# Kernel optimization log

Measured on AMD Instinct MI355X. Metric: run time of the kernel, lower is better.

The kernel has to match this reference:

```python
import jax, jax.numpy as jnp
import numpy as np

DIM = 512
CHUNK = 64
LN_EPS = 1e-5


def setup_inputs() -> dict:
    key = jax.random.key(0)
    ks = jax.random.split(key, 9)
    B, S, D = 4, 4096, DIM
    x = jax.random.normal(ks[0], (B, S, D), dtype=jnp.float32)
    # Linear weights stored as [in, out] (equivalent to torch W.T)
    W_omega = jax.random.normal(ks[1], (D, D), dtype=jnp.float32) / np.sqrt(D)
    b_omega = jnp.zeros((D,), dtype=jnp.float32)
    log_scale = jnp.full((D,), np.log(0.1), dtype=jnp.float32)
    ln_gamma = jnp.ones((4 * D,), dtype=jnp.float32)
    ln_beta = jnp.zeros((4 * D,), dtype=jnp.float32)
    W1 = jax.random.normal(ks[2], (4 * D, 2 * D), dtype=jnp.float32) / np.sqrt(4 * D)
    b1 = jnp.zeros((2 * D,), dtype=jnp.float32)
    W2 = jax.random.normal(ks[3], (2 * D, D), dtype=jnp.float32) / np.sqrt(2 * D)
    b2 = jnp.zeros((D,), dtype=jnp.float32)
    return {"x": x, "W_omega": W_omega, "b_omega": b_omega, "log_scale": log_scale,
            "ln_gamma": ln_gamma, "ln_beta": ln_beta, "W1": W1, "b1": b1, "W2": W2, "b2": b2}


def reference(x, W_omega, b_omega, log_scale, ln_gamma, ln_beta, W1, b1, W2, b2):
    B, S, D = x.shape
    C = CHUNK
    # S chosen as multiple of C, so pad_len == 0 (matches torch no-pad branch)
    N = S // C
    omega = x @ W_omega + b_omega                      # [B,S,D]
    oc = omega.reshape(B, N, C, D)
    xc = x.reshape(B, N, C, D)
    pos = jnp.arange(1, C + 1, dtype=x.dtype)          # [C]
    pos_scale = (1.0 / jnp.sqrt(pos))[None, None, :, None]
    scale = jnp.exp(log_scale)
    phi = jnp.cumsum(oc * scale * pos_scale, axis=2)   # [B,N,C,D]
    cos_phi = jnp.cos(phi)
    sin_phi = jnp.sin(phi)
    cr = xc * cos_phi                                   # content modulated real
    ci = xc * sin_phi                                   # content modulated imag
    pos_norm = pos[None, None, :, None]
    mr = jnp.cumsum(cr, axis=2) / pos_norm              # memory real
    mi = jnp.cumsum(ci, axis=2) / pos_norm              # memory imag
    rr = mr * cos_phi + mi * sin_phi                    # retrieved real
    ri = mi * cos_phi - mr * sin_phi                    # retrieved imag
    ctx = jnp.concatenate([cr.reshape(B, S, D), ci.reshape(B, S, D),
                           rr.reshape(B, S, D), ri.reshape(B, S, D)], axis=-1)  # [B,S,4D]
    mu = jnp.mean(ctx, axis=-1, keepdims=True)
    var = jnp.mean((ctx - mu) ** 2, axis=-1, keepdims=True)
    h = (ctx - mu) / jnp.sqrt(var + LN_EPS) * ln_gamma + ln_beta
    h = h @ W1 + b1
    h = jax.nn.gelu(h, approximate=False)               # torch GELU default = exact erf
    out = h @ W2 + b2                                   # dropout is identity at eval
    return x + out
```

## Files before the change

kernel.cpp:

```cpp
#include <hip/hip_runtime.h>
#include <hip/hip_bf16.h>
#include <math.h>


typedef __bf16 bf16x8 __attribute__((ext_vector_type(8)));
typedef __bf16 bf16x4 __attribute__((ext_vector_type(4)));
typedef __bf16 bf16x2 __attribute__((ext_vector_type(2)));
typedef float  f32x4  __attribute__((ext_vector_type(4)));

typedef __attribute__((address_space(1))) void* gas_ptr;
typedef __attribute__((address_space(3))) void* las_ptr;

__device__ __forceinline__ void load_lds16(const void* g, void* l) {
    __builtin_amdgcn_global_load_lds((gas_ptr)g, (las_ptr)l, 16, 0, 0);
}

__device__ __forceinline__ void transpose_tile(const float* __restrict__ in,
                                               __bf16* __restrict__ out,
                                               int K, int N, int bx, int by,
                                               float (*tile)[33])
{
    const int tid = threadIdx.x;
    const int tx = tid & 31, ty = tid >> 5;
    const int n0 = bx * 32, k0 = by * 32;
    #pragma unroll
    for (int i = 0; i < 32; i += 8)
        tile[ty + i][tx] = in[(size_t)(k0 + ty + i) * N + n0 + tx];
    __syncthreads();
    #pragma unroll
    for (int i = 0; i < 32; i += 8)
        out[(size_t)(n0 + ty + i) * K + k0 + tx] = (__bf16)tile[tx][ty + i];
}

__global__ __launch_bounds__(256)
void prep_kernel(const float* __restrict__ x, __bf16* __restrict__ xb,
                 const float* __restrict__ W_omega, __bf16* __restrict__ womT,
                 const float* __restrict__ W1, __bf16* __restrict__ w1T,
                 const float* __restrict__ W2, __bf16* __restrict__ w2T)
{
    __shared__ float tile[32][33];
    const int bid = blockIdx.x;
    if (bid < 8192) {
        int i = bid * 256 + threadIdx.x;
        float4 v = ((const float4*)x)[i];
        bf16x4 o = { (__bf16)v.x, (__bf16)v.y, (__bf16)v.z, (__bf16)v.w };
        ((bf16x4*)xb)[i] = o;
    } else if (bid < 8448) {
        int t = bid - 8192;
        transpose_tile(W_omega, womT, 512, 512, t & 15, t >> 4, tile);
    } else if (bid < 10496) {
        int t = bid - 8448;
        transpose_tile(W1, w1T, 2048, 1024, t & 31, t >> 5, tile);
    } else {
        int t = bid - 10496;
        transpose_tile(W2, w2T, 1024, 512, t & 15, t >> 4, tile);
    }
}

template<int MODE>
__global__ __launch_bounds__(256)
void gemm_kernel(const __bf16* __restrict__ A, const __bf16* __restrict__ Bt,
                 const float* __restrict__ bias, const __bf16* __restrict__ resid,
                 void* __restrict__ out, int M, int N, int K)
{
    __shared__ __bf16 As[2][128 * 64];
    __shared__ __bf16 Bs[2][128 * 64];

    const int tid     = threadIdx.x;
    const int tiles_n = N >> 7;
    const int ln_tn   = __ffs(tiles_n) - 1;
    const int per_m   = (M >> 7) >> 3;

    const int xcd = blockIdx.x & 7;
    const int j   = blockIdx.x >> 3;
    const int tile_m = (xcd * per_m + (j >> ln_tn)) << 7;
    const int tile_n = (j & (tiles_n - 1)) << 7;

    const int wave = tid >> 6;
    const int lane = tid & 63;

    const int srow = lane >> 3;
    const int scol = ((lane & 7) ^ srow) << 3;

    const __bf16* Ags = A  + (size_t)(tile_m + wave * 32 + srow) * K + scol;
    const __bf16* Bgs = Bt + (size_t)(tile_n + wave * 32 + srow) * K + scol;

    const int m0 = (wave >> 1) << 6;
    const int n0 = (wave & 1) << 6;
    const int lr = lane & 15;
    const int q  = lane >> 4;
    const int l7 = lane & 7;
    const int fc0 = ((0 + q) ^ l7) << 3;
    const int fc1 = ((4 + q) ^ l7) << 3;

    f32x4 acc[4][4];
    #pragma unroll
    for (int i = 0; i < 4; ++i)
        #pragma unroll
        for (int jj = 0; jj < 4; ++jj)
            acc[i][jj] = (f32x4){0.f, 0.f, 0.f, 0.f};

    const int nIter = K >> 6;

    #pragma unroll
    for (int c = 0; c < 4; ++c) {
        load_lds16(Ags + (size_t)(c * 8) * K, &As[0][(wave * 32 + c * 8) * 64]);
        load_lds16(Bgs + (size_t)(c * 8) * K, &Bs[0][(wave * 32 + c * 8) * 64]);
    }

    for (int it = 0; it < nIter; ++it) {
        const int cur = it & 1;
        __syncthreads();
        if (it + 1 < nIter) {
            const int nk = (it + 1) << 6;
            #pragma unroll
            for (int c = 0; c < 4; ++c) {
                load_lds16(Ags + nk + (size_t)(c * 8) * K, &As[cur ^ 1][(wave * 32 + c * 8) * 64]);
                load_lds16(Bgs + nk + (size_t)(c * 8) * K, &Bs[cur ^ 1][(wave * 32 + c * 8) * 64]);
            }
        }

        const __bf16* as = As[cur];
        const __bf16* bs = Bs[cur];
        {
            bf16x8 af[4], bq[4];
            #pragma unroll
            for (int i = 0; i < 4; ++i)
                af[i] = *(const bf16x8*)&as[(m0 + i * 16 + lr) * 64 + fc0];
            #pragma unroll
            for (int jj = 0; jj < 4; ++jj)
                bq[jj] = *(const bf16x8*)&bs[(n0 + jj * 16 + lr) * 64 + fc0];
            #pragma unroll
            for (int i = 0; i < 4; ++i)
                #pragma unroll
                for (int jj = 0; jj < 4; ++jj)
                    acc[i][jj] = __builtin_amdgcn_mfma_f32_16x16x32_bf16(af[i], bq[jj], acc[i][jj], 0, 0, 0);
        }
        {
            bf16x8 af[4], bq[4];
            #pragma unroll
            for (int i = 0; i < 4; ++i)
                af[i] = *(const bf16x8*)&as[(m0 + i * 16 + lr) * 64 + fc1];
            #pragma unroll
            for (int jj = 0; jj < 4; ++jj)
                bq[jj] = *(const bf16x8*)&bs[(n0 + jj * 16 + lr) * 64 + fc1];
            #pragma unroll
            for (int i = 0; i < 4; ++i)
                #pragma unroll
                for (int jj = 0; jj < 4; ++jj)
                    acc[i][jj] = __builtin_amdgcn_mfma_f32_16x16x32_bf16(af[i], bq[jj], acc[i][jj], 0, 0, 0);
        }
    }

    const int orow0 = tile_m + m0 + (q << 2);
    const int ocol0 = tile_n + n0 + lr;
    #pragma unroll
    for (int i = 0; i < 4; ++i) {
        #pragma unroll
        for (int jj = 0; jj < 4; ++jj) {
            const int col = ocol0 + jj * 16;
            const float bv = bias[col];
            #pragma unroll
            for (int r = 0; r < 4; ++r) {
                const int row = orow0 + i * 16 + r;
                float v = acc[i][jj][r] + bv;
                size_t idx = (size_t)row * N + col;
                if (MODE == 0) {
                    ((__bf16*)out)[idx] = (__bf16)v;
                } else if (MODE == 1) {
                    float g = 0.5f * v * (1.0f + erff(v * 0.70710678118654752f));
                    ((__bf16*)out)[idx] = (__bf16)g;
                } else {
                    ((float*)out)[idx] = v + (float)resid[idx];
                }
            }
        }
    }
}

__global__ __launch_bounds__(512)
void scan_ln_kernel(const __bf16* __restrict__ xb, const __bf16* __restrict__ omega,
                    const float* __restrict__ log_scale,
                    const float* __restrict__ gamma, const float* __restrict__ beta,
                    __bf16* __restrict__ ctx)
{
    const int chunk = blockIdx.x;
    const int d     = threadIdx.x;
    const int lane  = d & 63, wv = d >> 6;
    const size_t base = (size_t)chunk * 64 * 512;

    const float scale = expf(log_scale[d]);
    const float g0 = gamma[d], g1 = gamma[512 + d], g2 = gamma[1024 + d], g3 = gamma[1536 + d];
    const float e0 = beta[d],  e1 = beta[512 + d],  e2 = beta[1024 + d],  e3 = beta[1536 + d];

    float phi = 0.f, scr = 0.f, sci = 0.f;
    __shared__ float red[2][16];

    float om_n = (float)omega[base + d];
    float xv_n = (float)xb[base + d];

    for (int c = 0; c < 64; ++c) {
        const float om = om_n;
        const float xv = xv_n;
        if (c < 63) {
            om_n = (float)omega[base + (size_t)(c + 1) * 512 + d];
            xv_n = (float)xb[base + (size_t)(c + 1) * 512 + d];
        }
        phi += om * scale * rsqrtf((float)(c + 1));
        float sp, cp;
        __sincosf(phi, &sp, &cp);
        const float cr = xv * cp, ci = xv * sp;
        scr += cr; sci += ci;
        const float inv = 1.0f / (float)(c + 1);
        const float mr = scr * inv, mi = sci * inv;
        const float rr = mr * cp + mi * sp;
        const float ri = mi * cp - mr * sp;

        float s  = cr + ci + rr + ri;
        float s2 = cr * cr + ci * ci + rr * rr + ri * ri;
        #pragma unroll
        for (int o = 32; o > 0; o >>= 1) {
            s  += __shfl_down(s, o);
            s2 += __shfl_down(s2, o);
        }
        if (lane == 0) { red[c & 1][wv] = s; red[c & 1][8 + wv] = s2; }
        __syncthreads();
        float S = 0.f, S2 = 0.f;
        #pragma unroll
        for (int i = 0; i < 8; ++i) { S += red[c & 1][i]; S2 += red[c & 1][8 + i]; }
        const float mu   = S * (1.0f / 2048.0f);
        const float var  = S2 * (1.0f / 2048.0f) - mu * mu;
        const float rstd = rsqrtf(var + 1e-5f);

        const size_t ob = ((size_t)chunk * 64 + c) * 2048;
        ctx[ob + d]        = (__bf16)(((cr - mu) * rstd) * g0 + e0);
        ctx[ob + 512 + d]  = (__bf16)(((ci - mu) * rstd) * g1 + e1);
        ctx[ob + 1024 + d] = (__bf16)(((rr - mu) * rstd) * g2 + e2);
        ctx[ob + 1536 + d] = (__bf16)(((ri - mu) * rstd) * g3 + e3);
    }
}

extern "C" void kernel_launch(void* const* d_in, const int* in_sizes, int n_in,
                              void* d_out, int out_size, void* d_ws, size_t ws_size,
                              hipStream_t stream)
{
    const float* x         = (const float*)d_in[0];
    const float* W_omega   = (const float*)d_in[1];
    const float* b_omega   = (const float*)d_in[2];
    const float* log_scale = (const float*)d_in[3];
    const float* ln_gamma  = (const float*)d_in[4];
    const float* ln_beta   = (const float*)d_in[5];
    const float* W1        = (const float*)d_in[6];
    const float* b1        = (const float*)d_in[7];
    const float* W2        = (const float*)d_in[8];
    const float* b2        = (const float*)d_in[9];
    float* out = (float*)d_out;

    char* ws = (char*)d_ws;
    __bf16* xb    = (__bf16*)(ws);
    __bf16* womT  = (__bf16*)(ws + 16777216);
    __bf16* w1T   = (__bf16*)(ws + 17301504);
    __bf16* w2T   = (__bf16*)(ws + 21495808);
    __bf16* omega = (__bf16*)(ws + 22544384);
    __bf16* hbuf  = (__bf16*)(ws + 22544384);
    __bf16* ctx   = (__bf16*)(ws + 56098816);

    prep_kernel<<<11008, 256, 0, stream>>>(x, xb, W_omega, womT, W1, w1T, W2, w2T);

    gemm_kernel<0><<<512, 256, 0, stream>>>(xb, womT, b_omega, nullptr, omega, 16384, 512, 512);

    scan_ln_kernel<<<256, 512, 0, stream>>>(xb, omega, log_scale, ln_gamma, ln_beta, ctx);

    gemm_kernel<1><<<1024, 256, 0, stream>>>(ctx, w1T, b1, nullptr, hbuf, 16384, 1024, 2048);

    gemm_kernel<2><<<512, 256, 0, stream>>>(hbuf, w2T, b2, xb, out, 16384, 512, 1024);
}
```

Baseline: 274.4 us.

## Add 256x256-tile multistage bf16 GEMM kernel for the W1 projection

Adds a new GEMM kernel with 256x256 output tiles, 512 threads and a 4-slot LDS ring. It fills the ring with direct global-to-LDS loads, uses XOR-swizzled fragment reads and raises wave priority around the MFMA block. The kernel replaces the generic GEMM for the largest matmul (ctx times W1 with fused GELU) and launches exactly 256 blocks with an XCD-aware tile mapping. The goal is more operand reuse per LDS byte and better overlap of loads with MFMA work. The cost is 128KB of LDS per block, which allows only one block per CU, and much higher register pressure from the 8x4 accumulator tile.

```diff
diff --git a/kernel.cpp b/kernel.cpp
--- a/kernel.cpp
+++ b/kernel.cpp
@@ -178,6 +178,118 @@
     }
 }
 
+template<int MODE>
+__global__ __launch_bounds__(512, 2)
+void gemm256_kernel(const __bf16* __restrict__ A, const __bf16* __restrict__ Bt,
+                    const float* __restrict__ bias, void* __restrict__ out,
+                    int M, int N, int K)
+{
+    __shared__ __bf16 As[4][256 * 32];
+    __shared__ __bf16 Bs[4][256 * 32];
+
+    const int tid  = threadIdx.x;
+    const int wv   = tid >> 6;
+    const int lane = tid & 63;
+    const int wm   = wv >> 2;
+    const int wn   = wv & 3;
+
+    const int tiles_n = N >> 8;
+    const int ln_tn   = __ffs(tiles_n) - 1;
+    const int per_m   = (M >> 8) >> 3;
+
+    const int xcd = blockIdx.x & 7;
+    const int j   = blockIdx.x >> 3;
+    const int tile_m = (xcd * per_m + (j >> ln_tn)) << 8;
+    const int tile_n = (j & (tiles_n - 1)) << 8;
+
+    const int srow = 16 * wv + (lane >> 2);
+    const int sig8 = (((lane & 3) ^ ((lane >> 3) & 3)) << 3);
+
+    const __bf16* Ag = A  + (size_t)(tile_m + srow) * K + sig8;
+    const __bf16* Bg = Bt + (size_t)(tile_n + srow) * K + sig8;
+    const size_t rowK128 = (size_t)128 * K;
+    const int lbase = wv * 512;
+
+    const int lr    = lane & 15;
+    const int q4    = lane >> 4;
+    const int fslot = ((q4 ^ ((lane >> 1) & 3)) << 3);
+    const int arow0 = wm * 128 + lr;
+    const int brow0 = wn * 64 + lr;
+
+    f32x4 acc[8][4];
+    #pragma unroll
+    for (int i = 0; i < 8; ++i)
+        #pragma unroll
+        for (int jj = 0; jj < 4; ++jj)
+            acc[i][jj] = (f32x4){0.f, 0.f, 0.f, 0.f};
+
+    const int NKS = K >> 5;
+
+    auto stage = [&](int ks) {
+        const int slot = ks & 3;
+        const __bf16* ag = Ag + (ks << 5);
+        const __bf16* bg = Bg + (ks << 5);
+        load_lds16(ag,           &As[slot][lbase]);
+        load_lds16(ag + rowK128, &As[slot][4096 + lbase]);
+        load_lds16(bg,           &Bs[slot][lbase]);
+        load_lds16(bg + rowK128, &Bs[slot][4096 + lbase]);
+    };
+
+    if (0 < NKS) stage(0);
+    if (1 < NKS) stage(1);
+    if (2 < NKS) stage(2);
+
+    for (int ks = 0; ks < NKS; ++ks) {
+        if (ks + 2 < NKS)      asm volatile("s_waitcnt vmcnt(8)" ::: "memory");
+        else if (ks + 1 < NKS) asm volatile("s_waitcnt vmcnt(4)" ::: "memory");
+        else                   asm volatile("s_waitcnt vmcnt(0)" ::: "memory");
+        __builtin_amdgcn_s_barrier();
+        asm volatile("" ::: "memory");
+
+        if (ks + 3 < NKS) stage(ks + 3);
+
+        const __bf16* as = As[ks & 3];
+        const __bf16* bs = Bs[ks & 3];
+        bf16x8 af[8], bq[4];
+        #pragma unroll
+        for (int i = 0; i < 8; ++i)
+            af[i] = *(const bf16x8*)&as[(arow0 + i * 16) * 32 + fslot];
+        #pragma unroll
+        for (int jj = 0; jj < 4; ++jj)
+            bq[jj] = *(const bf16x8*)&bs[(brow0 + jj * 16) * 32 + fslot];
+
+        __builtin_amdgcn_s_setprio(1);
+        #pragma unroll
+        for (int i = 0; i < 8; ++i)
+            #pragma unroll
+            for (int jj = 0; jj < 4; ++jj)
+                acc[i][jj] = __builtin_amdgcn_mfma_f32_16x16x32_bf16(af[i], bq[jj], acc[i][jj], 0, 0, 0);
+        __builtin_amdgcn_s_setprio(0);
+    }
+
+    const int orow0 = tile_m + wm * 128 + (q4 << 2);
+    const int ocol0 = tile_n + wn * 64 + lr;
+    #pragma unroll
+    for (int i = 0; i < 8; ++i) {
+        #pragma unroll
+        for (int jj = 0; jj < 4; ++jj) {
+            const int col = ocol0 + jj * 16;
+            const float bv = bias[col];
+            #pragma unroll
+            for (int r = 0; r < 4; ++r) {
+                const int row = orow0 + i * 16 + r;
+                float v = acc[i][jj][r] + bv;
+                if (MODE == 1) {
+                    float g = 0.5f * v * (1.0f + erff(v * 0.70710678118654752f));
+                    ((__bf16*)out)[(size_t)row * N + col] = (__bf16)g;
+                } else {
+                    ((__bf16*)out)[(size_t)row * N + col] = (__bf16)v;
+                }
+            }
+        }
+    }
+}
+
 __global__ __launch_bounds__(512)
 void scan_ln_kernel(const __bf16* __restrict__ xb, const __bf16* __restrict__ omega,
                     const float* __restrict__ log_scale,
@@ -271,7 +383,7 @@
 
     scan_ln_kernel<<<256, 512, 0, stream>>>(xb, omega, log_scale, ln_gamma, ln_beta, ctx);
 
-    gemm_kernel<1><<<1024, 256, 0, stream>>>(ctx, w1T, b1, nullptr, hbuf, 16384, 1024, 2048);
+    gemm256_kernel<1><<<256, 512, 0, stream>>>(ctx, w1T, b1, hbuf, 16384, 1024, 2048);
 
     gemm_kernel<2><<<512, 256, 0, stream>>>(hbuf, w2T, b2, xb, out, 16384, 512, 1024);
 }
```

Result: slower. 285.1 us (+3.9%).

## Use 256x256-tile 512-thread GEMM with LDS double buffering for W1 projection

Applied to the files above, without the earlier changes.

Adds a new GEMM kernel with 256x256 output tiles, 8 waves per block, double-buffered global-to-LDS async loads with XOR swizzle, interleaved staging and MFMA phases, and XCD-aware tile mapping. It replaces the previous 128-tile GEMM for the large LN-to-W1 projection with fused GELU, aiming to raise arithmetic intensity and overlap loads with compute. The larger tile reduces the grid to 256 blocks at one block per CU, so occupancy is low and correctness depends on the hand-written swizzle and sync scheme.

```diff
diff --git a/kernel.cpp b/kernel.cpp
--- a/kernel.cpp
+++ b/kernel.cpp
@@ -178,6 +178,157 @@
     }
 }
 
+template<int MODE>
+__global__ __launch_bounds__(512, 1)
+void gemm256_kernel(const __bf16* __restrict__ A, const __bf16* __restrict__ Bt,
+                    const float* __restrict__ bias, void* __restrict__ out,
+                    int M, int N, int K)
+{
+    __shared__ __bf16 As[2 * 2 * 128 * 64];
+    __shared__ __bf16 Bs[2 * 2 * 128 * 64];
+
+    const int tid  = threadIdx.x;
+    const int wv   = tid >> 6;
+    const int lane = tid & 63;
+    const int wm   = wv >> 2;
+    const int wn   = wv & 3;
+
+    const int tiles_n = N >> 8;
+    const int ln_tn   = __ffs(tiles_n) - 1;
+    const int per_m   = (M >> 8) >> 3;
+
+    const int xcd = blockIdx.x & 7;
+    const int j   = blockIdx.x >> 3;
+    const int tile_m = (xcd * per_m + (j >> ln_tn)) << 8;
+    const int tile_n = (j & (tiles_n - 1)) << 8;
+
+    const int srow8 = lane >> 3;
+    const int sig8  = ((lane & 7) ^ srow8) << 3;
+    const __bf16* AgBase = A  + (size_t)(tile_m + wv * 8 + srow8) * K + sig8;
+    const __bf16* BgBase = Bt + (size_t)(tile_n + wv * 8 + srow8) * K + sig8;
+
+    const int lr = lane & 15;
+    const int q  = lane >> 4;
+    const unsigned ldsA0 = (unsigned)(size_t)(las_ptr)&As[0];
+    const unsigned ldsB0 = (unsigned)(size_t)(las_ptr)&Bs[0];
+    const unsigned chs   = (unsigned)((q ^ (lr & 7)) << 4);
+    const unsigned aA0b0 = ldsA0 + (unsigned)(wm * 16384 + lr * 128) + chs;
+    const unsigned aA1b0 = aA0b0 ^ 64;
+    const unsigned aA0b1 = aA0b0 + 32768;
+    const unsigned aA1b1 = aA1b0 + 32768;
+    const unsigned aB0b0 = ldsB0 + (unsigned)((wn >> 1) * 16384 + ((wn & 1) * 64 + lr) * 128) + chs;
+    const unsigned aB1b0 = aB0b0 ^ 64;
+    const unsigned aB0b1 = aB0b0 + 32768;
+    const unsigned aB1b1 = aB1b0 + 32768;
+
+    f32x4 acc[8][4];
+    #pragma unroll
+    for (int i = 0; i < 8; ++i)
+        #pragma unroll
+        for (int jj = 0; jj < 4; ++jj)
+            acc[i][jj] = (f32x4){0.f, 0.f, 0.f, 0.f};
+
+    const int NKT = K >> 6;
+
+    auto stageHalf = [&](int t, int op, int h) {
+        const size_t go = (size_t)(h * 128) * K + (size_t)(t << 6);
+        if (op == 0) {
+            __bf16* lb = As + (t & 1) * 16384 + h * 8192 + wv * 512;
+            load_lds16(AgBase + go, lb);
+            load_lds16(AgBase + go + (size_t)64 * K, lb + 4096);
+        } else {
+            __bf16* lb = Bs + (t & 1) * 16384 + h * 8192 + wv * 512;
+            load_lds16(BgBase + go, lb);
+            load_lds16(BgBase + go + (size_t)64 * K, lb + 4096);
+        }
+    };
+
+    bf16x8 afX[4], afY[4], bq0[4], bq1[4];
+
+#define DSR(d, a, o) asm volatile("ds_read_b128 %0, %1 offset:" o \
+                                  : "=v"(d) : "v"(a))
+
+#define PH_TAIL(AF, BQ, IB)                                                   \
+    asm volatile("s_waitcnt lgkmcnt(0)" ::: "memory");                        \
+    __builtin_amdgcn_sched_barrier(0);                                        \
+    __builtin_amdgcn_s_setprio(1);                                            \
+    _Pragma("unroll")                                                         \
+    for (int i_ = 0; i_ < 4; ++i_)                                            \
+        _Pragma("unroll")                                                     \
+        for (int j_ = 0; j_ < 4; ++j_)                                        \
+            acc[(IB) + i_][j_] = __builtin_amdgcn_mfma_f32_16x16x32_bf16(     \
+                AF[i_], BQ[j_], acc[(IB) + i_][j_], 0, 0, 0);                 \
+    __builtin_amdgcn_s_setprio(0);                                            \
+    __builtin_amdgcn_sched_barrier(0);
+
+#define GROUP(G, AK0, AK1, BK0, BK1)                                          \
+    {                                                                         \
+        asm volatile("s_waitcnt vmcnt(0)" ::: "memory");                      \
+        __builtin_amdgcn_s_barrier();                                         \
+        asm volatile("" ::: "memory");                                        \
+        const int tn_ = (G) + 1;                                              \
+        const bool st_ = tn_ < NKT;                                           \
+                                                                 \
+        if (st_) stageHalf(tn_, 0, 0);                                        \
+        DSR(afX[0], AK0, "0");    DSR(afX[1], AK0, "2048");                   \
+        DSR(afX[2], AK0, "4096"); DSR(afX[3], AK0, "6144");                   \
+        DSR(bq0[0], BK0, "0");    DSR(bq0[1], BK0, "2048");                   \
+        DSR(bq0[2], BK0, "4096"); DSR(bq0[3], BK0, "6144");                   \
+        PH_TAIL(afX, bq0, 0)                                                  \
+                                                                 \
+        if (st_) stageHalf(tn_, 0, 1);                                        \
+        DSR(afY[0], AK0, "8192");  DSR(afY[1], AK0, "10240");                 \
+        DSR(afY[2], AK0, "12288"); DSR(afY[3], AK0, "14336");                 \
+        PH_TAIL(afY, bq0, 4)                                                  \
+                                                                 \
+        if (st_) stageHalf(tn_, 1, 0);                                        \
+        DSR(afX[0], AK1, "0");    DSR(afX[1], AK1, "2048");                   \
+        DSR(afX[2], AK1, "4096"); DSR(afX[3], AK1, "6144");                   \
+        DSR(bq1[0], BK1, "0");    DSR(bq1[1], BK1, "2048");                   \
+        DSR(bq1[2], BK1, "4096"); DSR(bq1[3], BK1, "6144");                   \
+        PH_TAIL(afX, bq1, 0)                                                  \
+                                                                 \
+        if (st_) stageHalf(tn_, 1, 1);                                        \
+        DSR(afY[0], AK1, "8192");  DSR(afY[1], AK1, "10240");                 \
+        DSR(afY[2], AK1, "12288"); DSR(afY[3], AK1, "14336");                 \
+        PH_TAIL(afY, bq1, 4)                                                  \
+    }
+
+    stageHalf(0, 0, 0); stageHalf(0, 0, 1);
+    stageHalf(0, 1, 0); stageHalf(0, 1, 1);
+
+    for (int g = 0; g < NKT; g += 2) {
+        GROUP(g,     aA0b0, aA1b0, aB0b0, aB1b0)
+        GROUP(g + 1, aA0b1, aA1b1, aB0b1, aB1b1)
+    }
+
+#undef GROUP
+#undef PH_TAIL
+#undef DSR
+
+    const int orow0 = tile_m + wm * 128 + (q << 2);
+    const int ocol0 = tile_n + wn * 64 + lr;
+    #pragma unroll
+    for (int i = 0; i < 8; ++i) {
+        #pragma unroll
+        for (int jj = 0; jj < 4; ++jj) {
+            const int col = ocol0 + jj * 16;
+            const float bv = bias[col];
+            #pragma unroll
+            for (int r = 0; r < 4; ++r) {
+                const int row = orow0 + i * 16 + r;
+                float v = acc[i][jj][r] + bv;
+                if (MODE == 1) {
+                    float g = 0.5f * v * (1.0f + erff(v * 0.70710678118654752f));
+                    ((__bf16*)out)[(size_t)row * N + col] = (__bf16)g;
+                } else {
+                    ((__bf16*)out)[(size_t)row * N + col] = (__bf16)v;
+                }
+            }
+        }
+    }
+}
+
 __global__ __launch_bounds__(512)
 void scan_ln_kernel(const __bf16* __restrict__ xb, const __bf16* __restrict__ omega,
                     const float* __restrict__ log_scale,
@@ -271,7 +422,7 @@
 
     scan_ln_kernel<<<256, 512, 0, stream>>>(xb, omega, log_scale, ln_gamma, ln_beta, ctx);
 
-    gemm_kernel<1><<<1024, 256, 0, stream>>>(ctx, w1T, b1, nullptr, hbuf, 16384, 1024, 2048);
+    gemm256_kernel<1><<<256, 512, 0, stream>>>(ctx, w1T, b1, hbuf, 16384, 1024, 2048);
 
     gemm_kernel<2><<<512, 256, 0, stream>>>(hbuf, w2T, b2, xb, out, 16384, 512, 1024);
 }
```

New measurement: 262.6 us. 4.3% less time.
